# Kernel tuning notes

Measured on AMD Instinct MI355X. Metric: run time of the kernel, lower is better.

The kernel has to match this reference:

```python
import jax, jax.numpy as jnp
import numpy as np

ETYPES = ((0, 2), (4, 6))  # per-metapath edge-type indices into the doubled r_vec table
ALPHA = 3.0


def celu3(x):
    return jax.nn.celu(x, alpha=ALPHA)


def cmul(a, b):
    # complex multiply, last dim = (real, imag)
    re = a[..., 0] * b[..., 0] - a[..., 1] * b[..., 1]
    im = a[..., 0] * b[..., 1] + a[..., 1] * b[..., 0]
    return jnp.stack([re, im], axis=-1)


def setup_inputs() -> dict:
    key = jax.random.key(0)
    ks = jax.random.split(key, 10)
    N, H, heads, M, E, P = 50000, 64, 4, 2, 250000, 3
    R, FH = 4, 128
    D = heads * H
    return {
        "features": jax.random.normal(ks[0], (N, H), jnp.float32),
        "r_vec": jax.random.normal(ks[1], (R, H // 2, 2), jnp.float32),
        "attn1_w": jax.random.normal(ks[2], (heads, H), jnp.float32) * 0.1,
        "attn2": jax.random.normal(ks[3], (1, heads, H), jnp.float32) * 0.1,
        "fw1": jax.random.normal(ks[4], (2 * FH, D), jnp.float32) * 0.05,
        "fb1": jnp.zeros((2 * FH,), jnp.float32),
        "fw2": jax.random.normal(ks[5], (FH, 2 * FH), jnp.float32) * 0.05,
        "fb2": jnp.zeros((FH,), jnp.float32),
        "fw3": jax.random.normal(ks[6], (1, FH), jnp.float32) * 0.05,
        "instances": jax.random.randint(ks[7], (M, E, P), 0, N, jnp.int32),
    }


def reference(features, r_vec, attn1_w, attn2, fw1, fb1, fw2, fb2, fw3, instances):
    N, H = features.shape
    M, E, P = instances.shape
    heads = attn1_w.shape[0]
    # unit-modulus rotations + conjugates: [2R, H/2, 2], even=r, odd=conj(r)
    rv = r_vec / jnp.linalg.norm(r_vec, axis=2, keepdims=True)
    conj = rv * jnp.array([1.0, -1.0], rv.dtype)
    rv2 = jnp.stack([rv, conj], axis=1).reshape(-1, H // 2, 2)

    per_path = []
    for m in range(M):
        inst = instances[m]  # [E, P]
        # backward cumulative rotation: final_r[i] = prod_{j>=i} r_{etype[j]}, final_r[P-1]=1
        ident = jnp.stack([jnp.ones(H // 2, rv.dtype), jnp.zeros(H // 2, rv.dtype)], axis=-1)
        frs = [ident]
        for i in range(P - 2, -1, -1):
            frs.insert(0, cmul(frs[0], rv2[ETYPES[m][i]]))
        fr = jnp.stack(frs)  # [P, H/2, 2]
        # gather features along metapath and rotate (last position rotated by identity)
        edata = features[inst].reshape(E, P, H // 2, 2)
        rot = cmul(edata, fr[None])
        me = jnp.mean(rot.reshape(E, P, H), axis=1)  # [E, H]
        se = celu3(me) * jax.nn.sigmoid(me)  # gated metapath embedding
        eft = celu3(se)  # same across heads in original (tiled)
        seg = inst[:, 0]  # target node per instance
        a1 = celu3(features[seg] @ attn1_w.T)  # [E, heads]
        a2 = jnp.einsum('eh,kh->ek', eft, attn2[0])  # [E, heads]
        a = celu3(a1 + a2)
        # segment softmax over each node's instance set
        amax = jax.ops.segment_max(a, seg, num_segments=N)
        ex = jnp.exp(a - amax[seg])
        den = jax.ops.segment_sum(ex, seg, num_segments=N)
        attn = ex / den[seg]  # [E, heads]
        hsum = jax.ops.segment_sum(attn[:, :, None] * eft[:, None, :], seg, num_segments=N)
        per_path.append(celu3(hsum).reshape(N, heads * H))  # empty nodes -> 0

    z = jnp.stack(per_path, axis=1)  # [N, M, D]
    t = celu3(z @ fw1.T + fb1)
    t = celu3(t @ fw2.T + fb2)
    w = (t @ fw3.T).mean(axis=0)  # [M, 1]
    beta = jax.nn.softmax(w, axis=0)
    out = (beta * z).sum(axis=1)  # [N, D]
    return out
```

## Files before the change

kernel.cpp:

```cpp
#include <hip/hip_runtime.h>
#include <hip/hip_bf16.h>

typedef unsigned short u16;
typedef unsigned int   u32;
typedef short bf16x8 __attribute__((ext_vector_type(8)));
typedef float f32x4  __attribute__((ext_vector_type(4)));

#define CAP 64

__device__ inline float b2f(u16 u){ return __builtin_bit_cast(float, (u32)u << 16); }
__device__ inline u16 f2b(float f){
  u32 x = __builtin_bit_cast(u32, f);
  x += 0x7fffu + ((x >> 16) & 1u);
  return (u16)(x >> 16);
}
__device__ inline u32 pk2(float lo, float hi){
  float2 f; f.x = lo; f.y = hi;
  __hip_bfloat162 h = __float22bfloat162_rn(f);
  u32 r; __builtin_memcpy(&r, &h, 4);
  return r;
}
__device__ inline void up2(u32 u, float& lo, float& hi){
  lo = __builtin_bit_cast(float, u << 16);
  hi = __builtin_bit_cast(float, u & 0xffff0000u);
}
__device__ inline float fexp(float x){ return __expf(x); }
__device__ inline float frcp(float x){ return __builtin_amdgcn_rcpf(x); }
__device__ inline float celu3(float x){
  return x > 0.f ? x : 3.f * (__expf(x * (1.f/3.f)) - 1.f);
}
__device__ inline float act_chain(float x){
  float u  = __expf(x * (1.f/3.f));
  float u3 = u*u*u;
  float sg = u3 * frcp(u3 + 1.f);
  float c1 = x > 0.f ? x : 3.f*u - 3.f;
  float se = c1 * sg;
  return se > 0.f ? se : 3.f*__expf(se*(1.f/3.f)) - 3.f;
}

__global__ __launch_bounds__(256) void pre_kernel(
    const float* __restrict__ feat, const float* __restrict__ attn1,
    const float* __restrict__ rvec, const float* __restrict__ fw1,
    const float* __restrict__ fw2,
    u16* __restrict__ featb, u16* __restrict__ rotA, u16* __restrict__ rotB,
    float* __restrict__ a1c, u16* __restrict__ fw1b, u16* __restrict__ fw2b,
    int* __restrict__ cnt, float* __restrict__ wacc,
    int N, int nbA)
{
  __shared__ float w1s[256], rvs[256];
  int b = blockIdx.x, t = threadIdx.x;
  if (b >= nbA){
    int cb = b - nbA;
    if (cb < 48){
      const float* src = (cb < 32) ? fw1 : fw2;
      u16* dst = (cb < 32) ? fw1b : fw2b;
      int i = (cb < 32 ? cb : cb - 32)*256 + t;
      float4 a = ((const float4*)src)[2*i], bb = ((const float4*)src)[2*i + 1];
      uint4 o;
      o.x = pk2(a.x, a.y);  o.y = pk2(a.z, a.w);
      o.z = pk2(bb.x, bb.y); o.w = pk2(bb.z, bb.w);
      ((uint4*)dst)[i] = o;
      return;
    }
    cb -= 48;
    int i = cb*256 + t;
    if (i*4 < 2*N) ((uint4*)cnt)[i] = make_uint4(0u,0u,0u,0u);
    if (cb == 0 && t < 128) wacc[t] = 0.f;
    return;
  }
  w1s[t] = attn1[t];
  rvs[t] = rvec[t];
  __syncthreads();
  int g = t >> 4, l = t & 15;
  int n = b * 16 + g;
  if (n >= N) return;
  float4 x = ((const float4*)feat)[(size_t)n*16 + l];
  float4 xs;
  xs.x = x.x*(1.f/3.f); xs.y = x.y*(1.f/3.f);
  xs.z = x.z*(1.f/3.f); xs.w = x.w*(1.f/3.f);
  uint2 o;
  o.x = pk2(xs.x, xs.y);
  o.y = pk2(xs.z, xs.w);
  ((uint2*)featb)[(size_t)n*16 + l] = o;

  #pragma unroll
  for (int m = 0; m < 2; ++m){
    float4 ra = *(const float4*)&rvs[(2*m)*64 + l*4];
    float4 rb = *(const float4*)&rvs[(2*m+1)*64 + l*4];
    float na0 = rsqrtf(ra.x*ra.x + ra.y*ra.y); ra.x*=na0; ra.y*=na0;
    float na1 = rsqrtf(ra.z*ra.z + ra.w*ra.w); ra.z*=na1; ra.w*=na1;
    float nb0 = rsqrtf(rb.x*rb.x + rb.y*rb.y); rb.x*=nb0; rb.y*=nb0;
    float nb1 = rsqrtf(rb.z*rb.z + rb.w*rb.w); rb.z*=nb1; rb.w*=nb1;
    float A0r = rb.x*ra.x - rb.y*ra.y, A0i = rb.x*ra.y + rb.y*ra.x;
    float A1r = rb.z*ra.z - rb.w*ra.w, A1i = rb.z*ra.w + rb.w*ra.z;
    uint2 oa, ob;
    oa.x = pk2(xs.x*A0r - xs.y*A0i, xs.x*A0i + xs.y*A0r);
    oa.y = pk2(xs.z*A1r - xs.w*A1i, xs.z*A1i + xs.w*A1r);
    ob.x = pk2(xs.x*rb.x - xs.y*rb.y, xs.x*rb.y + xs.y*rb.x);
    ob.y = pk2(xs.z*rb.z - xs.w*rb.w, xs.z*rb.w + xs.w*rb.z);
    ((uint2*)rotA)[((size_t)m*N + n)*16 + l] = oa;
    ((uint2*)rotB)[((size_t)m*N + n)*16 + l] = ob;
  }

  float d[4];
  #pragma unroll
  for (int k = 0; k < 4; ++k){
    int wb = k*64 + l*4;
    d[k] = x.x*w1s[wb] + x.y*w1s[wb+1] + x.z*w1s[wb+2] + x.w*w1s[wb+3];
  }
  #pragma unroll
  for (int off = 8; off; off >>= 1){
    #pragma unroll
    for (int k = 0; k < 4; ++k) d[k] += __shfl_xor(d[k], off);
  }
  if (l == 0){
    float4 av;
    av.x = celu3(d[0]); av.y = celu3(d[1]);
    av.z = celu3(d[2]); av.w = celu3(d[3]);
    ((float4*)a1c)[n] = av;
  }
}

__global__ __launch_bounds__(256) void edge_kernel(
    const u16* __restrict__ rotA, const u16* __restrict__ rotB,
    const u16* __restrict__ featb, const int* __restrict__ inst,
    const float* __restrict__ a1c, const float* __restrict__ attn2,
    u16* __restrict__ eft, float* __restrict__ a_ws,
    int* __restrict__ cnt, int* __restrict__ bucket, int E, int N)
{
  __shared__ float w2s[256];
  int m = blockIdx.y;
  int t = threadIdx.x;
  w2s[t] = attn2[t];
  __syncthreads();

  int g = t >> 3, l = t & 7;
  int e = blockIdx.x * 32 + g;
  if (e >= E) return;
  int base = (m*E + e)*3;
  int i0 = inst[base], i1 = inst[base+1], i2 = inst[base+2];
  size_t mN = (size_t)m * N;

  uint4 v0 = ((const uint4*)rotA)[(mN + i0)*8 + l];
  uint4 v1 = ((const uint4*)rotB)[(mN + i1)*8 + l];
  uint4 v2 = ((const uint4*)featb)[(size_t)i2*8 + l];
  float A[8], B[8], C[8];
  up2(v0.x, A[0], A[1]); up2(v0.y, A[2], A[3]);
  up2(v0.z, A[4], A[5]); up2(v0.w, A[6], A[7]);
  up2(v1.x, B[0], B[1]); up2(v1.y, B[2], B[3]);
  up2(v1.z, B[4], B[5]); up2(v1.w, B[6], B[7]);
  up2(v2.x, C[0], C[1]); up2(v2.y, C[2], C[3]);
  up2(v2.z, C[4], C[5]); up2(v2.w, C[6], C[7]);

  float ef[8];
  #pragma unroll
  for (int c = 0; c < 8; ++c)
    ef[c] = act_chain(A[c] + B[c] + C[c]);

  uint4 uo;
  uo.x = pk2(ef[0], ef[1]);
  uo.y = pk2(ef[2], ef[3]);
  uo.z = pk2(ef[4], ef[5]);
  uo.w = pk2(ef[6], ef[7]);
  ((uint4*)eft)[(size_t)(m*E + e)*8 + l] = uo;

  float d2[4];
  #pragma unroll
  for (int k = 0; k < 4; ++k){
    int wb = k*64 + l*8;
    float4 wA = *(const float4*)&w2s[wb];
    float4 wB = *(const float4*)&w2s[wb+4];
    d2[k] = ef[0]*wA.x + ef[1]*wA.y + ef[2]*wA.z + ef[3]*wA.w
          + ef[4]*wB.x + ef[5]*wB.y + ef[6]*wB.z + ef[7]*wB.w;
  }
  #pragma unroll
  for (int off = 4; off; off >>= 1){
    #pragma unroll
    for (int k = 0; k < 4; ++k) d2[k] += __shfl_xor(d2[k], off);
  }
  if (l == 0){
    float4 a1v4 = ((const float4*)a1c)[i0];
    float4 av;
    av.x = celu3(a1v4.x + d2[0]);
    av.y = celu3(a1v4.y + d2[1]);
    av.z = celu3(a1v4.z + d2[2]);
    av.w = celu3(a1v4.w + d2[3]);
    ((float4*)a_ws)[m*E + e] = av;
    int pos = atomicAdd(&cnt[m*N + i0], 1);
    if (pos < CAP) bucket[(size_t)(m*N + i0)*CAP + pos] = e;
  }
}

__global__ __launch_bounds__(256) void seg_kernel(
    const float* __restrict__ a_ws, const u16* __restrict__ eft,
    const int* __restrict__ cnt, const int* __restrict__ bucket,
    u16* __restrict__ z, int E, int N)
{
  __shared__ float wls[4][64][4];
  __shared__ int   els[4][64];
  int wvb = threadIdx.x >> 6;
  int m = blockIdx.y;
  int n = blockIdx.x * 4 + wvb;
  if (n >= N) return;
  int lane = threadIdx.x & 63;
  int sidx = m*N + n;
  int deg = cnt[sidx]; if (deg > CAP) deg = CAP;

  float h0=0.f, h1=0.f, h2=0.f, h3=0.f;
  if (deg > 0){
    const int* bk = bucket + (size_t)sidx * CAP;
    size_t ebase = (size_t)m * E;

    int e = (lane < deg) ? bk[lane] : 0;
    float w0 = 0.f, w1 = 0.f, w2 = 0.f, w3 = 0.f;
    if (lane < deg){
      float4 av = ((const float4*)a_ws)[ebase + e];
      w0 = fexp(av.x); w1 = fexp(av.y); w2 = fexp(av.z); w3 = fexp(av.w);
    }
    els[wvb][lane] = e;
    *(float4*)&wls[wvb][lane][0] = make_float4(w0, w1, w2, w3);

    float d0=w0, d1=w1, d2=w2, d3=w3;
    #pragma unroll
    for (int off = 32; off; off >>= 1){
      d0 += __shfl_xor(d0, off); d1 += __shfl_xor(d1, off);
      d2 += __shfl_xor(d2, off); d3 += __shfl_xor(d3, off);
    }

    const u16* ep = eft + ebase*64 + lane;
    int j = 0;
    for (; j + 1 < deg; j += 2){
      int ej0 = els[wvb][j], ej1 = els[wvb][j+1];
      float4 wj0 = *(const float4*)&wls[wvb][j][0];
      float4 wj1 = *(const float4*)&wls[wvb][j+1][0];
      float ev0 = b2f(ep[(size_t)ej0*64]);
      float ev1 = b2f(ep[(size_t)ej1*64]);
      h0 += wj0.x*ev0; h1 += wj0.y*ev0; h2 += wj0.z*ev0; h3 += wj0.w*ev0;
      h0 += wj1.x*ev1; h1 += wj1.y*ev1; h2 += wj1.z*ev1; h3 += wj1.w*ev1;
    }
    if (j < deg){
      int ej0 = els[wvb][j];
      float4 wj0 = *(const float4*)&wls[wvb][j][0];
      float ev0 = b2f(ep[(size_t)ej0*64]);
      h0 += wj0.x*ev0; h1 += wj0.y*ev0; h2 += wj0.z*ev0; h3 += wj0.w*ev0;
    }
    h0 *= frcp(d0); h1 *= frcp(d1); h2 *= frcp(d2); h3 *= frcp(d3);
  }
  u16* zr = z + (size_t)sidx*256 + lane;
  zr[0]   = f2b(celu3(h0));
  zr[64]  = f2b(celu3(h1));
  zr[128] = f2b(celu3(h2));
  zr[192] = f2b(celu3(h3));
}

__global__ __launch_bounds__(512, 4) void mlp_kernel(
    const u16* __restrict__ z, const u16* __restrict__ fw1b, const float* __restrict__ fb1,
    const u16* __restrict__ fw2b, const float* __restrict__ fb2, const float* __restrict__ fw3,
    float* __restrict__ waccP, int rows, int N)
{
  __shared__ u16 buf[64][264];
  __shared__ float fw3s[128];
  __shared__ float sPart[8][64];
  int tid = threadIdx.x;
  int row0 = blockIdx.x * 64;
  int wv = tid >> 6, lane = tid & 63, lr = lane & 15, quad = lane >> 4;

  const uint4* zg = (const uint4*)z;
  uint4 zr4[4];
  #pragma unroll
  for (int it = 0; it < 4; ++it){
    int idx = it*512 + tid;
    int row = idx >> 5, c8 = idx & 31;
    int gr = row0 + row;
    zr4[it] = make_uint4(0u,0u,0u,0u);
    if (gr < rows) zr4[it] = zg[(size_t)gr*32 + c8];
  }

  const u16* wb1 = fw1b + (size_t)(wv*32 + lr)*256 + quad*8;
  bf16x8 B1[2][8];
  #pragma unroll
  for (int nt = 0; nt < 2; ++nt)
    #pragma unroll
    for (int ks = 0; ks < 8; ++ks)
      B1[nt][ks] = *(const bf16x8*)(wb1 + nt*16*256 + ks*32);

  if (tid < 128) fw3s[tid] = fw3[tid];

  #pragma unroll
  for (int it = 0; it < 4; ++it){
    int idx = it*512 + tid;
    int row = idx >> 5, c8 = idx & 31;
    *(uint4*)&buf[row][c8*8] = zr4[it];
  }
  __syncthreads();

  f32x4 zero4 = {0.f, 0.f, 0.f, 0.f};

  f32x4 acc[4][2];
  #pragma unroll
  for (int a = 0; a < 4; ++a){ acc[a][0] = zero4; acc[a][1] = zero4; }
  #pragma unroll
  for (int ks = 0; ks < 8; ++ks){
    #pragma unroll
    for (int mt = 0; mt < 4; ++mt){
      bf16x8 af = *(const bf16x8*)&buf[mt*16 + lr][ks*32 + quad*8];
      acc[mt][0] = __builtin_amdgcn_mfma_f32_16x16x32_bf16(af, B1[0][ks], acc[mt][0], 0, 0, 0);
      acc[mt][1] = __builtin_amdgcn_mfma_f32_16x16x32_bf16(af, B1[1][ks], acc[mt][1], 0, 0, 0);
    }
  }

  const u16* wb2 = fw2b + (size_t)(wv*16 + lr)*256 + quad*8;
  bf16x8 B2[8];
  #pragma unroll
  for (int ks = 0; ks < 8; ++ks)
    B2[ks] = *(const bf16x8*)(wb2 + ks*32);

  __syncthreads();
  #pragma unroll
  for (int nt = 0; nt < 2; ++nt){
    int col = wv*32 + nt*16 + lr;
    float bias = fb1[col];
    #pragma unroll
    for (int mt = 0; mt < 4; ++mt)
      #pragma unroll
      for (int ri = 0; ri < 4; ++ri){
        int row = mt*16 + quad*4 + ri;
        buf[row][col] = f2b(celu3(acc[mt][nt][ri] + bias));
      }
  }
  __syncthreads();

  f32x4 acc2[4];
  #pragma unroll
  for (int a = 0; a < 4; ++a) acc2[a] = zero4;
  #pragma unroll
  for (int ks = 0; ks < 8; ++ks){
    #pragma unroll
    for (int mt = 0; mt < 4; ++mt){
      bf16x8 af = *(const bf16x8*)&buf[mt*16 + lr][ks*32 + quad*8];
      acc2[mt] = __builtin_amdgcn_mfma_f32_16x16x32_bf16(af, B2[ks], acc2[mt], 0, 0, 0);
    }
  }

  {
    int col = wv*16 + lr;
    float bias2 = fb2[col];
    float w3 = fw3s[col];
    float ps[4][4];
    #pragma unroll
    for (int mt = 0; mt < 4; ++mt)
      #pragma unroll
      for (int ri = 0; ri < 4; ++ri)
        ps[mt][ri] = celu3(acc2[mt][ri] + bias2) * w3;
    #pragma unroll
    for (int off = 8; off; off >>= 1)
      #pragma unroll
      for (int mt = 0; mt < 4; ++mt)
        #pragma unroll
        for (int ri = 0; ri < 4; ++ri)
          ps[mt][ri] += __shfl_xor(ps[mt][ri], off);
    if (lr == 0){
      #pragma unroll
      for (int mt = 0; mt < 4; ++mt)
        #pragma unroll
        for (int ri = 0; ri < 4; ++ri)
          sPart[wv][mt*16 + quad*4 + ri] = ps[mt][ri];
    }
  }
  __syncthreads();

  if (tid < 64){
    float s = 0.f;
    #pragma unroll
    for (int w = 0; w < 8; ++w) s += sPart[w][tid];
    int gr = row0 + tid;
    if (gr >= rows) s = 0.f;
    float s0 = (gr < N) ? s : 0.f;
    float s1 = (gr < N) ? 0.f : s;
    #pragma unroll
    for (int off = 32; off; off >>= 1){
      s0 += __shfl_xor(s0, off);
      s1 += __shfl_xor(s1, off);
    }
    if (tid == 0){
      int slot = blockIdx.x & 63;
      atomicAdd(&waccP[slot],      s0);
      atomicAdd(&waccP[64 + slot], s1);
    }
  }
}

__global__ __launch_bounds__(256) void out_kernel(
    const u16* __restrict__ z, const float* __restrict__ wacc,
    float* __restrict__ out, int total, float invN)
{
  __shared__ float bsh[2];
  int tid = threadIdx.x;
  if (tid < 64){
    float s0 = wacc[tid], s1 = wacc[64 + tid];
    #pragma unroll
    for (int off = 32; off; off >>= 1){
      s0 += __shfl_xor(s0, off);
      s1 += __shfl_xor(s1, off);
    }
    if (tid == 0){
      float w0 = s0*invN, w1 = s1*invN;
      float mx = fmaxf(w0, w1);
      float e0 = __expf(w0 - mx), e1 = __expf(w1 - mx);
      float s = e0 + e1;
      bsh[0] = e0 / s;
      bsh[1] = e1 / s;
    }
  }
  __syncthreads();
  float b0 = bsh[0], b1 = bsh[1];
  int idx = blockIdx.x * 256 + tid;
  if (idx*8 >= total) return;
  uint4 u0 = ((const uint4*)z)[idx];
  uint4 u1 = ((const uint4*)z)[(total >> 3) + idx];
  float a0,a1v,c0,c1;
  float4 o;
  up2(u0.x, a0, a1v); up2(u1.x, c0, c1);
  o.x = b0*a0 + b1*c0; o.y = b0*a1v + b1*c1;
  up2(u0.y, a0, a1v); up2(u1.y, c0, c1);
  o.z = b0*a0 + b1*c0; o.w = b0*a1v + b1*c1;
  ((float4*)out)[idx*2] = o;
  up2(u0.z, a0, a1v); up2(u1.z, c0, c1);
  o.x = b0*a0 + b1*c0; o.y = b0*a1v + b1*c1;
  up2(u0.w, a0, a1v); up2(u1.w, c0, c1);
  o.z = b0*a0 + b1*c0; o.w = b0*a1v + b1*c1;
  ((float4*)out)[idx*2 + 1] = o;
}

extern "C" void kernel_launch(void* const* d_in, const int* in_sizes, int n_in,
                              void* d_out, int out_size, void* d_ws, size_t ws_size,
                              hipStream_t stream)
{
  (void)n_in; (void)out_size; (void)ws_size;
  const float* feat  = (const float*)d_in[0];
  const float* rvec  = (const float*)d_in[1];
  const float* attn1 = (const float*)d_in[2];
  const float* attn2 = (const float*)d_in[3];
  const float* fw1   = (const float*)d_in[4];
  const float* fb1   = (const float*)d_in[5];
  const float* fw2   = (const float*)d_in[6];
  const float* fb2   = (const float*)d_in[7];
  const float* fw3   = (const float*)d_in[8];
  const int*   inst  = (const int*)d_in[9];

  int N = in_sizes[0] / 64;
  int E = in_sizes[9] / 6;

  char* ws = (char*)d_ws;
  u16*   z      = (u16*)ws;                            size_t zB = (size_t)2*N*256*2;
  u16*   eft    = (u16*)(ws + zB);                     size_t eB = (size_t)2*E*64*2;
  float* a_ws   = (float*)(ws + zB + eB);              size_t aB = (size_t)2*E*4*4;
  int*   bucket = (int*)(ws + zB + eB + aB);           size_t bB = (size_t)2*N*CAP*4;
  int*   cnt    = (int*)(ws + zB + eB + aB + bB);      size_t cB = (size_t)2*N*4;
  u16*   featb  = (u16*)(ws + zB + eB + aB + bB + cB); size_t fB = (size_t)N*64*2;
  float* a1c    = (float*)(ws + zB + eB + aB + bB + cB + fB);  size_t a1B = (size_t)N*4*4;
  u16*   fw1b   = (u16*)(ws + zB + eB + aB + bB + cB + fB + a1B);
  u16*   fw2b   = fw1b + 256*256;
  float* wacc   = (float*)(fw2b + 128*256);

  u16* rotA = z;
  u16* rotB = z + (size_t)2*N*64;

  int nbA = (N + 15)/16;
  int nbZ = ((2*N)/4 + 255)/256;
  pre_kernel<<<nbA + 48 + nbZ, 256, 0, stream>>>(
      feat, attn1, rvec, fw1, fw2, featb, rotA, rotB, a1c, fw1b, fw2b,
      cnt, wacc, N, nbA);
  edge_kernel<<<dim3((E + 31)/32, 2), 256, 0, stream>>>(
      rotA, rotB, featb, inst, a1c, attn2, eft, a_ws, cnt, bucket, E, N);
  seg_kernel<<<dim3((N + 3)/4, 2), 256, 0, stream>>>(a_ws, eft, cnt, bucket, z, E, N);
  mlp_kernel<<<(2*N + 63)/64, 512, 0, stream>>>(z, fw1b, fb1, fw2b, fb2, fw3, wacc, 2*N, N);
  out_kernel<<<((N*256/8) + 255)/256, 256, 0, stream>>>(z, wacc, (float*)d_out, N*256, 1.f/(float)N);
}
```

Before: 270.9 us.

## Persistent MLP kernel with prefetch, two edges per thread, deeper seg unroll

The MLP kernel becomes persistent on a fixed grid of 512 blocks. Each block keeps its fw1 B-fragments in registers across tiles and prefetches the next tile's z rows while the current tile's MFMAs run. The edge kernel handles two edges per thread group so more gathers are in flight, and the seg kernel's aggregation loop is unrolled by four for more memory-level parallelism. In exchange, register pressure goes up (launch bounds lowered to 2 blocks) and the fixed grid may not match the CU count.

```diff
diff --git a/kernel.cpp b/kernel.cpp
--- a/kernel.cpp
+++ b/kernel.cpp
@@ -135,59 +135,98 @@
   __syncthreads();
 
   int g = t >> 3, l = t & 7;
-  int e = blockIdx.x * 32 + g;
-  if (e >= E) return;
-  int base = (m*E + e)*3;
-  int i0 = inst[base], i1 = inst[base+1], i2 = inst[base+2];
+  int e0 = blockIdx.x * 64 + g;
+  int e1 = e0 + 32;
+  bool ok0 = e0 < E, ok1 = e1 < E;
+  int ec0 = ok0 ? e0 : 0, ec1 = ok1 ? e1 : 0;
   size_t mN = (size_t)m * N;
-
-  uint4 v0 = ((const uint4*)rotA)[(mN + i0)*8 + l];
-  uint4 v1 = ((const uint4*)rotB)[(mN + i1)*8 + l];
-  uint4 v2 = ((const uint4*)featb)[(size_t)i2*8 + l];
-  float A[8], B[8], C[8];
-  up2(v0.x, A[0], A[1]); up2(v0.y, A[2], A[3]);
-  up2(v0.z, A[4], A[5]); up2(v0.w, A[6], A[7]);
-  up2(v1.x, B[0], B[1]); up2(v1.y, B[2], B[3]);
-  up2(v1.z, B[4], B[5]); up2(v1.w, B[6], B[7]);
-  up2(v2.x, C[0], C[1]); up2(v2.y, C[2], C[3]);
-  up2(v2.z, C[4], C[5]); up2(v2.w, C[6], C[7]);
-
-  float ef[8];
-  #pragma unroll
-  for (int c = 0; c < 8; ++c)
-    ef[c] = act_chain(A[c] + B[c] + C[c]);
-
-  uint4 uo;
-  uo.x = pk2(ef[0], ef[1]);
-  uo.y = pk2(ef[2], ef[3]);
-  uo.z = pk2(ef[4], ef[5]);
-  uo.w = pk2(ef[6], ef[7]);
-  ((uint4*)eft)[(size_t)(m*E + e)*8 + l] = uo;
-
-  float d2[4];
+  size_t mE = (size_t)m * E;
+
+  int b0 = (int)((mE + ec0)*3), b1 = (int)((mE + ec1)*3);
+  int i00 = inst[b0], i01 = inst[b0+1], i02 = inst[b0+2];
+  int i10 = inst[b1], i11 = inst[b1+1], i12 = inst[b1+2];
+
+  uint4 v00 = ((const uint4*)rotA)[(mN + i00)*8 + l];
+  uint4 v01 = ((const uint4*)rotB)[(mN + i01)*8 + l];
+  uint4 v02 = ((const uint4*)featb)[(size_t)i02*8 + l];
+  uint4 v10 = ((const uint4*)rotA)[(mN + i10)*8 + l];
+  uint4 v11 = ((const uint4*)rotB)[(mN + i11)*8 + l];
+  uint4 v12 = ((const uint4*)featb)[(size_t)i12*8 + l];
+
+  float A[8], B[8], C[8], ef0[8], ef1[8];
+  up2(v00.x, A[0], A[1]); up2(v00.y, A[2], A[3]);
+  up2(v00.z, A[4], A[5]); up2(v00.w, A[6], A[7]);
+  up2(v01.x, B[0], B[1]); up2(v01.y, B[2], B[3]);
+  up2(v01.z, B[4], B[5]); up2(v01.w, B[6], B[7]);
+  up2(v02.x, C[0], C[1]); up2(v02.y, C[2], C[3]);
+  up2(v02.z, C[4], C[5]); up2(v02.w, C[6], C[7]);
+  #pragma unroll
+  for (int c = 0; c < 8; ++c) ef0[c] = act_chain(A[c] + B[c] + C[c]);
+
+  up2(v10.x, A[0], A[1]); up2(v10.y, A[2], A[3]);
+  up2(v10.z, A[4], A[5]); up2(v10.w, A[6], A[7]);
+  up2(v11.x, B[0], B[1]); up2(v11.y, B[2], B[3]);
+  up2(v11.z, B[4], B[5]); up2(v11.w, B[6], B[7]);
+  up2(v12.x, C[0], C[1]); up2(v12.y, C[2], C[3]);
+  up2(v12.z, C[4], C[5]); up2(v12.w, C[6], C[7]);
+  #pragma unroll
+  for (int c = 0; c < 8; ++c) ef1[c] = act_chain(A[c] + B[c] + C[c]);
+
+  if (ok0){
+    uint4 uo;
+    uo.x = pk2(ef0[0], ef0[1]); uo.y = pk2(ef0[2], ef0[3]);
+    uo.z = pk2(ef0[4], ef0[5]); uo.w = pk2(ef0[6], ef0[7]);
+    ((uint4*)eft)[(mE + e0)*8 + l] = uo;
+  }
+  if (ok1){
+    uint4 uo;
+    uo.x = pk2(ef1[0], ef1[1]); uo.y = pk2(ef1[2], ef1[3]);
+    uo.z = pk2(ef1[4], ef1[5]); uo.w = pk2(ef1[6], ef1[7]);
+    ((uint4*)eft)[(mE + e1)*8 + l] = uo;
+  }
+
+  float d20[4], d21[4];
   #pragma unroll
   for (int k = 0; k < 4; ++k){
     int wb = k*64 + l*8;
     float4 wA = *(const float4*)&w2s[wb];
     float4 wB = *(const float4*)&w2s[wb+4];
-    d2[k] = ef[0]*wA.x + ef[1]*wA.y + ef[2]*wA.z + ef[3]*wA.w
-          + ef[4]*wB.x + ef[5]*wB.y + ef[6]*wB.z + ef[7]*wB.w;
+    d20[k] = ef0[0]*wA.x + ef0[1]*wA.y + ef0[2]*wA.z + ef0[3]*wA.w
+           + ef0[4]*wB.x + ef0[5]*wB.y + ef0[6]*wB.z + ef0[7]*wB.w;
+    d21[k] = ef1[0]*wA.x + ef1[1]*wA.y + ef1[2]*wA.z + ef1[3]*wA.w
+           + ef1[4]*wB.x + ef1[5]*wB.y + ef1[6]*wB.z + ef1[7]*wB.w;
   }
   #pragma unroll
   for (int off = 4; off; off >>= 1){
     #pragma unroll
-    for (int k = 0; k < 4; ++k) d2[k] += __shfl_xor(d2[k], off);
+    for (int k = 0; k < 4; ++k){
+      d20[k] += __shfl_xor(d20[k], off);
+      d21[k] += __shfl_xor(d21[k], off);
+    }
   }
   if (l == 0){
-    float4 a1v4 = ((const float4*)a1c)[i0];
-    float4 av;
-    av.x = celu3(a1v4.x + d2[0]);
-    av.y = celu3(a1v4.y + d2[1]);
-    av.z = celu3(a1v4.z + d2[2]);
-    av.w = celu3(a1v4.w + d2[3]);
-    ((float4*)a_ws)[m*E + e] = av;
-    int pos = atomicAdd(&cnt[m*N + i0], 1);
-    if (pos < CAP) bucket[(size_t)(m*N + i0)*CAP + pos] = e;
+    if (ok0){
+      float4 a1v4 = ((const float4*)a1c)[i00];
+      float4 av;
+      av.x = celu3(a1v4.x + d20[0]);
+      av.y = celu3(a1v4.y + d20[1]);
+      av.z = celu3(a1v4.z + d20[2]);
+      av.w = celu3(a1v4.w + d20[3]);
+      ((float4*)a_ws)[mE + e0] = av;
+      int pos = atomicAdd(&cnt[m*N + i00], 1);
+      if (pos < CAP) bucket[(size_t)(m*N + i00)*CAP + pos] = e0;
+    }
+    if (ok1){
+      float4 a1v4 = ((const float4*)a1c)[i10];
+      float4 av;
+      av.x = celu3(a1v4.x + d21[0]);
+      av.y = celu3(a1v4.y + d21[1]);
+      av.z = celu3(a1v4.z + d21[2]);
+      av.w = celu3(a1v4.w + d21[3]);
+      ((float4*)a_ws)[mE + e1] = av;
+      int pos = atomicAdd(&cnt[m*N + i10], 1);
+      if (pos < CAP) bucket[(size_t)(m*N + i10)*CAP + pos] = e1;
+    }
   }
 }
 
@@ -229,16 +268,23 @@
 
     const u16* ep = eft + ebase*64 + lane;
     int j = 0;
-    for (; j + 1 < deg; j += 2){
-      int ej0 = els[wvb][j], ej1 = els[wvb][j+1];
+    for (; j + 3 < deg; j += 4){
+      int ej0 = els[wvb][j],   ej1 = els[wvb][j+1];
+      int ej2 = els[wvb][j+2], ej3 = els[wvb][j+3];
+      float ev0 = b2f(ep[(size_t)ej0*64]);
+      float ev1 = b2f(ep[(size_t)ej1*64]);
+      float ev2 = b2f(ep[(size_t)ej2*64]);
+      float ev3 = b2f(ep[(size_t)ej3*64]);
       float4 wj0 = *(const float4*)&wls[wvb][j][0];
       float4 wj1 = *(const float4*)&wls[wvb][j+1][0];
-      float ev0 = b2f(ep[(size_t)ej0*64]);
-      float ev1 = b2f(ep[(size_t)ej1*64]);
+      float4 wj2 = *(const float4*)&wls[wvb][j+2][0];
+      float4 wj3 = *(const float4*)&wls[wvb][j+3][0];
       h0 += wj0.x*ev0; h1 += wj0.y*ev0; h2 += wj0.z*ev0; h3 += wj0.w*ev0;
       h0 += wj1.x*ev1; h1 += wj1.y*ev1; h2 += wj1.z*ev1; h3 += wj1.w*ev1;
-    }
-    if (j < deg){
+      h0 += wj2.x*ev2; h1 += wj2.y*ev2; h2 += wj2.z*ev2; h3 += wj2.w*ev2;
+      h0 += wj3.x*ev3; h1 += wj3.y*ev3; h2 += wj3.z*ev3; h3 += wj3.w*ev3;
+    }
+    for (; j < deg; ++j){
       int ej0 = els[wvb][j];
       float4 wj0 = *(const float4*)&wls[wvb][j][0];
       float ev0 = b2f(ep[(size_t)ej0*64]);
@@ -253,7 +299,7 @@
   zr[192] = f2b(celu3(h3));
 }
 
-__global__ __launch_bounds__(512, 4) void mlp_kernel(
+__global__ __launch_bounds__(512, 2) void mlp_kernel(
     const u16* __restrict__ z, const u16* __restrict__ fw1b, const float* __restrict__ fb1,
     const u16* __restrict__ fw2b, const float* __restrict__ fb2, const float* __restrict__ fw3,
     float* __restrict__ waccP, int rows, int N)
@@ -262,19 +308,8 @@
   __shared__ float fw3s[128];
   __shared__ float sPart[8][64];
   int tid = threadIdx.x;
-  int row0 = blockIdx.x * 64;
   int wv = tid >> 6, lane = tid & 63, lr = lane & 15, quad = lane >> 4;
-
-  const uint4* zg = (const uint4*)z;
-  uint4 zr4[4];
-  #pragma unroll
-  for (int it = 0; it < 4; ++it){
-    int idx = it*512 + tid;
-    int row = idx >> 5, c8 = idx & 31;
-    int gr = row0 + row;
-    zr4[it] = make_uint4(0u,0u,0u,0u);
-    if (gr < rows) zr4[it] = zg[(size_t)gr*32 + c8];
-  }
+  f32x4 zero4 = {0.f, 0.f, 0.f, 0.f};
 
   const u16* wb1 = fw1b + (size_t)(wv*32 + lr)*256 + quad*8;
   bf16x8 B1[2][8];
@@ -283,110 +318,152 @@
     #pragma unroll
     for (int ks = 0; ks < 8; ++ks)
       B1[nt][ks] = *(const bf16x8*)(wb1 + nt*16*256 + ks*32);
-
+  #pragma unroll
+  for (int nt = 0; nt < 2; ++nt)
+    #pragma unroll
+    for (int ks = 0; ks < 8; ++ks)
+      asm volatile("" :: "v"(B1[nt][ks]));
+
+  const u16* wb2 = fw2b + (size_t)(wv*16 + lr)*256 + quad*8;
   if (tid < 128) fw3s[tid] = fw3[tid];
 
-  #pragma unroll
-  for (int it = 0; it < 4; ++it){
-    int idx = it*512 + tid;
-    int row = idx >> 5, c8 = idx & 31;
-    *(uint4*)&buf[row][c8*8] = zr4[it];
-  }
-  __syncthreads();
-
-  f32x4 zero4 = {0.f, 0.f, 0.f, 0.f};
-
-  f32x4 acc[4][2];
-  #pragma unroll
-  for (int a = 0; a < 4; ++a){ acc[a][0] = zero4; acc[a][1] = zero4; }
-  #pragma unroll
-  for (int ks = 0; ks < 8; ++ks){
-    #pragma unroll
-    for (int mt = 0; mt < 4; ++mt){
-      bf16x8 af = *(const bf16x8*)&buf[mt*16 + lr][ks*32 + quad*8];
-      acc[mt][0] = __builtin_amdgcn_mfma_f32_16x16x32_bf16(af, B1[0][ks], acc[mt][0], 0, 0, 0);
-      acc[mt][1] = __builtin_amdgcn_mfma_f32_16x16x32_bf16(af, B1[1][ks], acc[mt][1], 0, 0, 0);
-    }
-  }
-
-  const u16* wb2 = fw2b + (size_t)(wv*16 + lr)*256 + quad*8;
-  bf16x8 B2[8];
-  #pragma unroll
-  for (int ks = 0; ks < 8; ++ks)
-    B2[ks] = *(const bf16x8*)(wb2 + ks*32);
-
-  __syncthreads();
-  #pragma unroll
-  for (int nt = 0; nt < 2; ++nt){
-    int col = wv*32 + nt*16 + lr;
-    float bias = fb1[col];
-    #pragma unroll
-    for (int mt = 0; mt < 4; ++mt)
-      #pragma unroll
-      for (int ri = 0; ri < 4; ++ri){
-        int row = mt*16 + quad*4 + ri;
-        buf[row][col] = f2b(celu3(acc[mt][nt][ri] + bias));
+  const uint4* zg = (const uint4*)z;
+  int ntiles = (rows + 63) >> 6;
+  int gstride = gridDim.x;
+  int tile = blockIdx.x;
+
+  uint4 zr4[4];
+  {
+    int row0 = tile * 64;
+    #pragma unroll
+    for (int it = 0; it < 4; ++it){
+      int idx = it*512 + tid;
+      int row = idx >> 5, c8 = idx & 31;
+      int gr = row0 + row;
+      zr4[it] = make_uint4(0u,0u,0u,0u);
+      if (gr < rows) zr4[it] = zg[(size_t)gr*32 + c8];
+    }
+  }
+
+  for (; tile < ntiles; ){
+    int row0 = tile * 64;
+    #pragma unroll
+    for (int it = 0; it < 4; ++it){
+      int idx = it*512 + tid;
+      int row = idx >> 5, c8 = idx & 31;
+      *(uint4*)&buf[row][c8*8] = zr4[it];
+    }
+    __syncthreads();
+
+    int tnext = tile + gstride;
+    uint4 zn[4];
+    {
+      int nrow0 = tnext * 64;
+      #pragma unroll
+      for (int it = 0; it < 4; ++it){
+        int idx = it*512 + tid;
+        int row = idx >> 5, c8 = idx & 31;
+        int gr = nrow0 + row;
+        zn[it] = make_uint4(0u,0u,0u,0u);
+        if (tnext < ntiles && gr < rows) zn[it] = zg[(size_t)gr*32 + c8];
       }
-  }
-  __syncthreads();
-
-  f32x4 acc2[4];
-  #pragma unroll
-  for (int a = 0; a < 4; ++a) acc2[a] = zero4;
-  #pragma unroll
-  for (int ks = 0; ks < 8; ++ks){
-    #pragma unroll
-    for (int mt = 0; mt < 4; ++mt){
-      bf16x8 af = *(const bf16x8*)&buf[mt*16 + lr][ks*32 + quad*8];
-      acc2[mt] = __builtin_amdgcn_mfma_f32_16x16x32_bf16(af, B2[ks], acc2[mt], 0, 0, 0);
-    }
-  }
-
-  {
-    int col = wv*16 + lr;
-    float bias2 = fb2[col];
-    float w3 = fw3s[col];
-    float ps[4][4];
-    #pragma unroll
-    for (int mt = 0; mt < 4; ++mt)
-      #pragma unroll
-      for (int ri = 0; ri < 4; ++ri)
-        ps[mt][ri] = celu3(acc2[mt][ri] + bias2) * w3;
-    #pragma unroll
-    for (int off = 8; off; off >>= 1)
+    }
+
+    f32x4 acc[4][2];
+    #pragma unroll
+    for (int a = 0; a < 4; ++a){ acc[a][0] = zero4; acc[a][1] = zero4; }
+    #pragma unroll
+    for (int ks = 0; ks < 8; ++ks){
+      #pragma unroll
+      for (int mt = 0; mt < 4; ++mt){
+        bf16x8 af = *(const bf16x8*)&buf[mt*16 + lr][ks*32 + quad*8];
+        acc[mt][0] = __builtin_amdgcn_mfma_f32_16x16x32_bf16(af, B1[0][ks], acc[mt][0], 0, 0, 0);
+        acc[mt][1] = __builtin_amdgcn_mfma_f32_16x16x32_bf16(af, B1[1][ks], acc[mt][1], 0, 0, 0);
+      }
+    }
+
+    bf16x8 B2[8];
+    #pragma unroll
+    for (int ks = 0; ks < 8; ++ks)
+      B2[ks] = *(const bf16x8*)(wb2 + ks*32);
+
+    __syncthreads();
+    #pragma unroll
+    for (int nt = 0; nt < 2; ++nt){
+      int col = wv*32 + nt*16 + lr;
+      float bias = fb1[col];
+      #pragma unroll
+      for (int mt = 0; mt < 4; ++mt)
+        #pragma unroll
+        for (int ri = 0; ri < 4; ++ri){
+          int row = mt*16 + quad*4 + ri;
+          buf[row][col] = f2b(celu3(acc[mt][nt][ri] + bias));
+        }
+    }
+    __syncthreads();
+
+    f32x4 acc2[4];
+    #pragma unroll
+    for (int a = 0; a < 4; ++a) acc2[a] = zero4;
+    #pragma unroll
+    for (int ks = 0; ks < 8; ++ks){
+      #pragma unroll
+      for (int mt = 0; mt < 4; ++mt){
+        bf16x8 af = *(const bf16x8*)&buf[mt*16 + lr][ks*32 + quad*8];
+        acc2[mt] = __builtin_amdgcn_mfma_f32_16x16x32_bf16(af, B2[ks], acc2[mt], 0, 0, 0);
+      }
+    }
+
+    {
+      int col = wv*16 + lr;
+      float bias2 = fb2[col];
+      float w3 = fw3s[col];
+      float ps[4][4];
       #pragma unroll
       for (int mt = 0; mt < 4; ++mt)
         #pragma unroll
         for (int ri = 0; ri < 4; ++ri)
-          ps[mt][ri] += __shfl_xor(ps[mt][ri], off);
-    if (lr == 0){
-      #pragma unroll
-      for (int mt = 0; mt < 4; ++mt)
+          ps[mt][ri] = celu3(acc2[mt][ri] + bias2) * w3;
+      #pragma unroll
+      for (int off = 8; off; off >>= 1)
         #pragma unroll
-        for (int ri = 0; ri < 4; ++ri)
-          sPart[wv][mt*16 + quad*4 + ri] = ps[mt][ri];
-    }
-  }
-  __syncthreads();
-
-  if (tid < 64){
-    float s = 0.f;
-    #pragma unroll
-    for (int w = 0; w < 8; ++w) s += sPart[w][tid];
-    int gr = row0 + tid;
-    if (gr >= rows) s = 0.f;
-    float s0 = (gr < N) ? s : 0.f;
-    float s1 = (gr < N) ? 0.f : s;
-    #pragma unroll
-    for (int off = 32; off; off >>= 1){
-      s0 += __shfl_xor(s0, off);
-      s1 += __shfl_xor(s1, off);
-    }
-    if (tid == 0){
-      int slot = blockIdx.x & 63;
-      atomicAdd(&waccP[slot],      s0);
-      atomicAdd(&waccP[64 + slot], s1);
-    }
+        for (int mt = 0; mt < 4; ++mt)
+          #pragma unroll
+          for (int ri = 0; ri < 4; ++ri)
+            ps[mt][ri] += __shfl_xor(ps[mt][ri], off);
+      if (lr == 0){
+        #pragma unroll
+        for (int mt = 0; mt < 4; ++mt)
+          #pragma unroll
+          for (int ri = 0; ri < 4; ++ri)
+            sPart[wv][mt*16 + quad*4 + ri] = ps[mt][ri];
+      }
+    }
+    __syncthreads();
+
+    if (tid < 64){
+      float s = 0.f;
+      #pragma unroll
+      for (int w = 0; w < 8; ++w) s += sPart[w][tid];
+      int gr = row0 + tid;
+      if (gr >= rows) s = 0.f;
+      float s0 = (gr < N) ? s : 0.f;
+      float s1 = (gr < N) ? 0.f : s;
+      #pragma unroll
+      for (int off = 32; off; off >>= 1){
+        s0 += __shfl_xor(s0, off);
+        s1 += __shfl_xor(s1, off);
+      }
+      if (tid == 0){
+        int slot = tile & 63;
+        atomicAdd(&waccP[slot],      s0);
+        atomicAdd(&waccP[64 + slot], s1);
+      }
+    }
+
+    #pragma unroll
+    for (int it = 0; it < 4; ++it) zr4[it] = zn[it];
+    tile = tnext;
   }
 }
 
@@ -471,9 +548,9 @@
   pre_kernel<<<nbA + 48 + nbZ, 256, 0, stream>>>(
       feat, attn1, rvec, fw1, fw2, featb, rotA, rotB, a1c, fw1b, fw2b,
       cnt, wacc, N, nbA);
-  edge_kernel<<<dim3((E + 31)/32, 2), 256, 0, stream>>>(
+  edge_kernel<<<dim3((E + 63)/64, 2), 256, 0, stream>>>(
       rotA, rotB, featb, inst, a1c, attn2, eft, a_ws, cnt, bucket, E, N);
   seg_kernel<<<dim3((N + 3)/4, 2), 256, 0, stream>>>(a_ws, eft, cnt, bucket, z, E, N);
-  mlp_kernel<<<(2*N + 63)/64, 512, 0, stream>>>(z, fw1b, fb1, fw2b, fb2, fw3, wacc, 2*N, N);
+  mlp_kernel<<<512, 512, 0, stream>>>(z, fw1b, fb1, fw2b, fb2, fw3, wacc, 2*N, N);
   out_kernel<<<((N*256/8) + 255)/256, 256, 0, stream>>>(z, wacc, (float*)d_out, N*256, 1.f/(float)N);
 }
```

Result: no change. 266.8 us (-1.5%).
